# Kernel tuning notes

Hardware: AMD Instinct MI355X
Metric: run time of the kernel (lower is better)

## Reference

```python
import jax, jax.numpy as jnp
import numpy as np

B, T, D = 16, 4096, 1024
UNITS = 1024


def setup_inputs() -> dict:
    key = jax.random.key(0)
    ks = jax.random.split(key, 8)
    s_in = 1.0 / np.sqrt(D)
    s_u = 1.0 / np.sqrt(UNITS)
    return {
        "hidden_state": jax.random.normal(ks[0], (B, D), jnp.float32),
        "encoder_output": jax.random.normal(ks[1], (B, T, D), jnp.float32),
        "W1": jax.random.normal(ks[2], (D, UNITS), jnp.float32) * s_in,
        "b1": jnp.zeros((UNITS,), jnp.float32),
        "W2": jax.random.normal(ks[3], (D, UNITS), jnp.float32) * s_in,
        "b2": jnp.zeros((UNITS,), jnp.float32),
        "V": jax.random.normal(ks[4], (UNITS, 1), jnp.float32) * s_u,
        "bv": jnp.zeros((1,), jnp.float32),
    }


def reference(hidden_state, encoder_output, W1, b1, W2, b2, V, bv):
    # Bahdanau additive attention: score = V(tanh(W1(h) + W2(enc)))
    h_proj = hidden_state @ W1 + b1                      # [B, U]
    e_proj = jnp.einsum("btd,du->btu", encoder_output, W2) + b2  # [B, T, U]
    feat = jnp.tanh(h_proj[:, None, :] + e_proj)          # [B, T, U]
    score = feat @ V + bv                                 # [B, T, 1]
    attention_weights = jax.nn.softmax(score, axis=1)     # [B, T, 1]
    context_vector = jnp.sum(attention_weights * encoder_output, axis=1)  # [B, D]
    return context_vector, attention_weights
```

## Files before the change

kernel.cpp:

```cpp
#include <hip/hip_runtime.h>
#include <hip/hip_bf16.h>
#include <math.h>

#define B_ 16
#define T_ 4096
#define D_ 1024
#define U_ 1024
#define M_ (B_*T_)

typedef __attribute__((ext_vector_type(8))) short short8;
typedef __attribute__((ext_vector_type(4))) short short4v;
typedef __attribute__((ext_vector_type(4))) float float4v;

static __device__ __forceinline__ short f2bf(float f) {
    unsigned u = __builtin_bit_cast(unsigned, f);
    u += 0x7FFFu + ((u >> 16) & 1u);
    return (short)(u >> 16);
}
static __device__ __forceinline__ float bf2f(short s) {
    unsigned u = ((unsigned)(unsigned short)s) << 16;
    return __builtin_bit_cast(float, u);
}
static __device__ __forceinline__ float fast_tanh(float x) {
    float c = fminf(fmaxf(2.f * x, -30.f), 30.f);
    float t = __expf(c);
    return __fdividef(t - 1.f, t + 1.f);
}

#define GLLDS(GP, LP) __builtin_amdgcn_global_load_lds( \
    (const __attribute__((address_space(1))) void*)(GP), \
    (__attribute__((address_space(3))) void*)(LP), 16, 0, 0)

__global__ void hb_kernel(const float* __restrict__ h, const float* __restrict__ W1,
                          const float* __restrict__ b1, const float* __restrict__ b2,
                          float* __restrict__ hbp) {
    int x = blockIdx.x;
    int kc = x >> 6;
    int gid = (x & 63) * 256 + threadIdx.x;
    int b = gid >> 10, u = gid & 1023;
    const float* hr = h + b * D_ + kc * 256;
    const float* w = W1 + (size_t)(kc * 256) * U_ + u;
    float s0 = 0.f, s1 = 0.f, s2 = 0.f, s3 = 0.f;
    for (int k = 0; k < 256; k += 4) {
        s0 += hr[k+0] * w[(size_t)(k+0) * U_];
        s1 += hr[k+1] * w[(size_t)(k+1) * U_];
        s2 += hr[k+2] * w[(size_t)(k+2) * U_];
        s3 += hr[k+3] * w[(size_t)(k+3) * U_];
    }
    float s = ((s0 + s1) + (s2 + s3));
    if (kc == 0) s += b1[u] + b2[u];
    hbp[kc * 16384 + gid] = s;
}

__global__ void convert_enc(const float* __restrict__ enc, short* __restrict__ encbf) {
    size_t g = (size_t)blockIdx.x * 256 + threadIdx.x;
    const float4v* p = (const float4v*)(enc + g * 16);
    float4v f0 = p[0], f1 = p[1], f2 = p[2], f3 = p[3];
    short8 a, b;
    a[0]=f2bf(f0[0]); a[1]=f2bf(f0[1]); a[2]=f2bf(f0[2]); a[3]=f2bf(f0[3]);
    a[4]=f2bf(f1[0]); a[5]=f2bf(f1[1]); a[6]=f2bf(f1[2]); a[7]=f2bf(f1[3]);
    b[0]=f2bf(f2[0]); b[1]=f2bf(f2[1]); b[2]=f2bf(f2[2]); b[3]=f2bf(f2[3]);
    b[4]=f2bf(f3[0]); b[5]=f2bf(f3[1]); b[6]=f2bf(f3[2]); b[7]=f2bf(f3[3]);
    short8* q = (short8*)(encbf + g * 16);
    q[0] = a; q[1] = b;
}

__global__ void convert_w2t(const float* __restrict__ W2, short* __restrict__ W2T) {
    __shared__ short t[64][65];
    int k0 = (blockIdx.x >> 4) * 64, u0 = (blockIdx.x & 15) * 64;
    int tx = threadIdx.x & 63, ty = threadIdx.x >> 6;
    #pragma unroll
    for (int r = 0; r < 16; ++r) {
        int kk = ty * 16 + r;
        t[kk][tx] = f2bf(W2[(size_t)(k0 + kk) * U_ + u0 + tx]);
    }
    __syncthreads();
    #pragma unroll
    for (int r = 0; r < 16; ++r) {
        int uu = ty * 16 + r;
        W2T[(size_t)(u0 + uu) * D_ + k0 + tx] = t[tx][uu];
    }
}

__global__ __launch_bounds__(256) void gemm_score_bf16(
    const short* __restrict__ Abf,
    const short* __restrict__ W2T,
    const float* __restrict__ hbp,
    const float* __restrict__ V,
    float* __restrict__ scorepart)
{
    __shared__ __align__(16) short As[128 * 32];
    __shared__ __align__(16) short Bs[128 * 32];
    __shared__ float sbuf[2][128];

    const int tid = threadIdx.x;
    const int ntile = blockIdx.x, mtile = blockIdx.y;
    const int row0 = mtile * 128, n0 = ntile * 128;
    const int bidx = row0 >> 12;

    const int lane = tid & 63, wv = tid >> 6;
    const int wm = wv >> 1, wn = wv & 1;
    const int lm = lane & 15, quad = lane >> 4;
    const int arow = tid >> 2, akq = (tid & 3) * 8;

    float4v acc[4][4] = {};

    for (int K0 = 0; K0 < D_; K0 += 32) {
        GLLDS(Abf + (size_t)(row0 + arow) * D_ + K0 + akq,       As + tid * 8);
        GLLDS(Abf + (size_t)(row0 + 64 + arow) * D_ + K0 + akq,  As + 2048 + tid * 8);
        GLLDS(W2T + (size_t)(n0 + arow) * D_ + K0 + akq,         Bs + tid * 8);
        GLLDS(W2T + (size_t)(n0 + 64 + arow) * D_ + K0 + akq,    Bs + 2048 + tid * 8);
        __syncthreads();
        short8 af[4], bfr[4];
        #pragma unroll
        for (int mi = 0; mi < 4; ++mi)
            af[mi] = *(const short8*)&As[(wm * 64 + mi * 16 + lm) * 32 + quad * 8];
        #pragma unroll
        for (int ni = 0; ni < 4; ++ni)
            bfr[ni] = *(const short8*)&Bs[(wn * 64 + ni * 16 + lm) * 32 + quad * 8];
        #pragma unroll
        for (int mi = 0; mi < 4; ++mi)
            #pragma unroll
            for (int ni = 0; ni < 4; ++ni)
                acc[mi][ni] = __builtin_amdgcn_mfma_f32_16x16x32_bf16(
                    af[mi], bfr[ni], acc[mi][ni], 0, 0, 0);
        __syncthreads();
    }

    float hbv[4], Vv[4];
    #pragma unroll
    for (int ni = 0; ni < 4; ++ni) {
        int U = n0 + wn * 64 + ni * 16 + lm;
        int o = bidx * U_ + U;
        hbv[ni] = hbp[o] + hbp[16384 + o] + hbp[32768 + o] + hbp[49152 + o];
        Vv[ni]  = V[U];
    }
    #pragma unroll
    for (int mi = 0; mi < 4; ++mi) {
        #pragma unroll
        for (int r = 0; r < 4; ++r) {
            float s = 0.f;
            #pragma unroll
            for (int ni = 0; ni < 4; ++ni)
                s += fast_tanh(acc[mi][ni][r] + hbv[ni]) * Vv[ni];
            #pragma unroll
            for (int off = 1; off < 16; off <<= 1)
                s += __shfl_xor(s, off, 64);
            if (lm == 0)
                sbuf[wn][wm * 64 + mi * 16 + quad * 4 + r] = s;
        }
    }
    __syncthreads();
    if (tid < 128)
        scorepart[(size_t)ntile * M_ + row0 + tid] = sbuf[0][tid] + sbuf[1][tid];
}

__global__ void softmax_kernel(const float* __restrict__ scorepart,
                               const float* __restrict__ bv,
                               float* __restrict__ out_attn) {
    __shared__ float sm[T_];
    __shared__ float red[4];
    int b = blockIdx.x, tid = threadIdx.x;
    float bvv = bv[0];
    float lmax = -1e30f;
    for (int i = 0; i < 16; ++i) {
        int t = tid + i * 256;
        float s = bvv;
        #pragma unroll
        for (int p = 0; p < 8; ++p) s += scorepart[(size_t)p * M_ + b * T_ + t];
        sm[t] = s;
        lmax = fmaxf(lmax, s);
    }
    #pragma unroll
    for (int off = 1; off < 64; off <<= 1) lmax = fmaxf(lmax, __shfl_xor(lmax, off, 64));
    int wv = tid >> 6;
    if ((tid & 63) == 0) red[wv] = lmax;
    __syncthreads();
    lmax = fmaxf(fmaxf(red[0], red[1]), fmaxf(red[2], red[3]));
    float lsum = 0.f;
    for (int i = 0; i < 16; ++i) {
        int t = tid + i * 256;
        float e = __expf(sm[t] - lmax);
        sm[t] = e;
        lsum += e;
    }
    #pragma unroll
    for (int off = 1; off < 64; off <<= 1) lsum += __shfl_xor(lsum, off, 64);
    __syncthreads();
    if ((tid & 63) == 0) red[wv] = lsum;
    __syncthreads();
    float rinv = 1.f / ((red[0] + red[1]) + (red[2] + red[3]));
    for (int i = 0; i < 16; ++i) {
        int t = tid + i * 256;
        out_attn[b * T_ + t] = sm[t] * rinv;
    }
}

__global__ void ctx_part_bf(const short* __restrict__ encbf,
                            const float* __restrict__ attn,
                            float* __restrict__ part) {
    __shared__ float wsm[256];
    int x = blockIdx.x;
    int b = x & 15, tc = x >> 4;
    int tid = threadIdx.x;
    wsm[tid] = attn[b * T_ + tc * 256 + tid];
    __syncthreads();
    const short* e0 = encbf + (size_t)(b * T_ + tc * 256) * D_ + tid * 4;
    float4v acc = {};
    for (int t = 0; t < 256; ++t) {
        short4v v = *(const short4v*)(e0 + (size_t)t * D_);
        float w = wsm[t];
        acc[0] += w * bf2f(v[0]);
        acc[1] += w * bf2f(v[1]);
        acc[2] += w * bf2f(v[2]);
        acc[3] += w * bf2f(v[3]);
    }
    *(float4v*)(part + (size_t)x * 1024 + tid * 4) = acc;
}

__global__ void ctx_reduce_kernel(const float* __restrict__ part, float* __restrict__ ctx) {
    int gid = blockIdx.x * 256 + threadIdx.x;
    int b = gid >> 10, d = gid & 1023;
    float s = 0.f;
    #pragma unroll
    for (int tc = 0; tc < 16; ++tc) s += part[(size_t)(tc * 16 + b) * 1024 + d];
    ctx[gid] = s;
}

extern "C" void kernel_launch(void* const* d_in, const int* in_sizes, int n_in,
                              void* d_out, int out_size, void* d_ws, size_t ws_size,
                              hipStream_t stream) {
    const float* h   = (const float*)d_in[0];
    const float* enc = (const float*)d_in[1];
    const float* W1  = (const float*)d_in[2];
    const float* b1  = (const float*)d_in[3];
    const float* W2  = (const float*)d_in[4];
    const float* b2  = (const float*)d_in[5];
    const float* V   = (const float*)d_in[6];
    const float* bv  = (const float*)d_in[7];
    float* out = (float*)d_out;
    float* ws  = (float*)d_ws;

    float* hbp       = ws;
    float* scorepart = ws + 65536;
    float* ctxpart   = ws + 65536 + 524288;
    const size_t base_bytes = (65536 + 524288 + 262144) * 4;
    short* W2T   = (short*)((char*)d_ws + base_bytes);
    short* encbf = (short*)((char*)d_ws + base_bytes + (size_t)U_ * D_ * 2);

    hb_kernel<<<256, 256, 0, stream>>>(h, W1, b1, b2, hbp);
    convert_enc<<<16384, 256, 0, stream>>>(enc, encbf);
    convert_w2t<<<256, 256, 0, stream>>>(W2, W2T);
    gemm_score_bf16<<<dim3(8, 512), 256, 0, stream>>>(encbf, W2T, hbp, V, scorepart);
    softmax_kernel<<<16, 256, 0, stream>>>(scorepart, bv, out + 16384);
    ctx_part_bf<<<256, 256, 0, stream>>>(encbf, out + 16384, ctxpart);
    ctx_reduce_kernel<<<64, 256, 0, stream>>>(ctxpart, out);
}
```

Baseline: 622.4 us.

## Swizzle GEMM block order, widen softmax blocks, split context reduction finer

Remaps the GEMM's 1D grid so groups of 8 consecutive blocks share an M-tile set across N-tiles, aiming for better L2 reuse of A and W2T tiles. The softmax kernel now runs 1024 threads per batch row instead of 256, and the context partial kernel uses 128-timestep chunks over 512 blocks to expose more parallelism. The workspace reuses the score buffer for context partials, which is only safe because softmax finishes reading it before ctx_part writes.

```diff
diff --git a/kernel.cpp b/kernel.cpp
--- a/kernel.cpp
+++ b/kernel.cpp
@@ -94,7 +94,10 @@
     __shared__ float sbuf[2][128];
 
     const int tid = threadIdx.x;
-    const int ntile = blockIdx.x, mtile = blockIdx.y;
+    const int g = blockIdx.x;
+    const int c = g & 7, q = g >> 3;
+    const int ntile = q & 7;
+    const int mtile = (q >> 3) * 8 + c;
     const int row0 = mtile * 128, n0 = ntile * 128;
     const int bidx = row0 >> 12;
 
@@ -155,16 +158,20 @@
         scorepart[(size_t)ntile * M_ + row0 + tid] = sbuf[0][tid] + sbuf[1][tid];
 }
 
-__global__ void softmax_kernel(const float* __restrict__ scorepart,
-                               const float* __restrict__ bv,
-                               float* __restrict__ out_attn) {
+__global__ __launch_bounds__(1024) void softmax_kernel(
+        const float* __restrict__ scorepart,
+        const float* __restrict__ bv,
+        float* __restrict__ out_attn) {
     __shared__ float sm[T_];
-    __shared__ float red[4];
+    __shared__ float redm[16];
+    __shared__ float reds[16];
     int b = blockIdx.x, tid = threadIdx.x;
+    int wv = tid >> 6;
     float bvv = bv[0];
     float lmax = -1e30f;
-    for (int i = 0; i < 16; ++i) {
-        int t = tid + i * 256;
+    #pragma unroll
+    for (int i = 0; i < 4; ++i) {
+        int t = tid + i * 1024;
         float s = bvv;
         #pragma unroll
         for (int p = 0; p < 8; ++p) s += scorepart[(size_t)p * M_ + b * T_ + t];
@@ -173,25 +180,30 @@
     }
     #pragma unroll
     for (int off = 1; off < 64; off <<= 1) lmax = fmaxf(lmax, __shfl_xor(lmax, off, 64));
-    int wv = tid >> 6;
-    if ((tid & 63) == 0) red[wv] = lmax;
-    __syncthreads();
-    lmax = fmaxf(fmaxf(red[0], red[1]), fmaxf(red[2], red[3]));
+    if ((tid & 63) == 0) redm[wv] = lmax;
+    __syncthreads();
+    float m = redm[0];
+    #pragma unroll
+    for (int j = 1; j < 16; ++j) m = fmaxf(m, redm[j]);
     float lsum = 0.f;
-    for (int i = 0; i < 16; ++i) {
-        int t = tid + i * 256;
-        float e = __expf(sm[t] - lmax);
+    #pragma unroll
+    for (int i = 0; i < 4; ++i) {
+        int t = tid + i * 1024;
+        float e = __expf(sm[t] - m);
         sm[t] = e;
         lsum += e;
     }
     #pragma unroll
     for (int off = 1; off < 64; off <<= 1) lsum += __shfl_xor(lsum, off, 64);
-    __syncthreads();
-    if ((tid & 63) == 0) red[wv] = lsum;
-    __syncthreads();
-    float rinv = 1.f / ((red[0] + red[1]) + (red[2] + red[3]));
-    for (int i = 0; i < 16; ++i) {
-        int t = tid + i * 256;
+    if ((tid & 63) == 0) reds[wv] = lsum;
+    __syncthreads();
+    float tot = 0.f;
+    #pragma unroll
+    for (int j = 0; j < 16; ++j) tot += reds[j];
+    float rinv = 1.f / tot;
+    #pragma unroll
+    for (int i = 0; i < 4; ++i) {
+        int t = tid + i * 1024;
         out_attn[b * T_ + t] = sm[t] * rinv;
     }
 }
@@ -199,15 +211,15 @@
 __global__ void ctx_part_bf(const short* __restrict__ encbf,
                             const float* __restrict__ attn,
                             float* __restrict__ part) {
-    __shared__ float wsm[256];
+    __shared__ float wsm[128];
     int x = blockIdx.x;
     int b = x & 15, tc = x >> 4;
     int tid = threadIdx.x;
-    wsm[tid] = attn[b * T_ + tc * 256 + tid];
-    __syncthreads();
-    const short* e0 = encbf + (size_t)(b * T_ + tc * 256) * D_ + tid * 4;
+    if (tid < 128) wsm[tid] = attn[b * T_ + tc * 128 + tid];
+    __syncthreads();
+    const short* e0 = encbf + (size_t)(b * T_ + tc * 128) * D_ + tid * 4;
     float4v acc = {};
-    for (int t = 0; t < 256; ++t) {
+    for (int t = 0; t < 128; ++t) {
         short4v v = *(const short4v*)(e0 + (size_t)t * D_);
         float w = wsm[t];
         acc[0] += w * bf2f(v[0]);
@@ -223,7 +235,7 @@
     int b = gid >> 10, d = gid & 1023;
     float s = 0.f;
     #pragma unroll
-    for (int tc = 0; tc < 16; ++tc) s += part[(size_t)(tc * 16 + b) * 1024 + d];
+    for (int tc = 0; tc < 32; ++tc) s += part[(size_t)(tc * 16 + b) * 1024 + d];
     ctx[gid] = s;
 }
 
@@ -243,16 +255,15 @@
 
     float* hbp       = ws;
     float* scorepart = ws + 65536;
-    float* ctxpart   = ws + 65536 + 524288;
-    const size_t base_bytes = (65536 + 524288 + 262144) * 4;
-    short* W2T   = (short*)((char*)d_ws + base_bytes);
-    short* encbf = (short*)((char*)d_ws + base_bytes + (size_t)U_ * D_ * 2);
+    float* ctxpart   = scorepart;
+    short* W2T   = (short*)(ws + 65536 + 524288);
+    short* encbf = (short*)((char*)W2T + (size_t)U_ * D_ * 2);
 
     hb_kernel<<<256, 256, 0, stream>>>(h, W1, b1, b2, hbp);
     convert_enc<<<16384, 256, 0, stream>>>(enc, encbf);
     convert_w2t<<<256, 256, 0, stream>>>(W2, W2T);
-    gemm_score_bf16<<<dim3(8, 512), 256, 0, stream>>>(encbf, W2T, hbp, V, scorepart);
-    softmax_kernel<<<16, 256, 0, stream>>>(scorepart, bv, out + 16384);
-    ctx_part_bf<<<256, 256, 0, stream>>>(encbf, out + 16384, ctxpart);
+    gemm_score_bf16<<<4096, 256, 0, stream>>>(encbf, W2T, hbp, V, scorepart);
+    softmax_kernel<<<16, 1024, 0, stream>>>(scorepart, bv, out + 16384);
+    ctx_part_bf<<<512, 256, 0, stream>>>(encbf, out + 16384, ctxpart);
     ctx_reduce_kernel<<<64, 256, 0, stream>>>(ctxpart, out);
 }
```

Result: faster. 605.3 us (-2.7%).
